# Performance work log

Measured on AMD Instinct MI355X. Metric: run time of the kernel, lower is better.

The kernel has to match this reference:

```python
import jax, jax.numpy as jnp
import numpy as np
from jax import lax

H = 512   # hidden_size
R = 4     # read heads
W = 32    # memory word size
N = 64    # memory cells
B = 64    # batch
T = 256   # seq len
IFACE = R * W + 3 * W + 5 * R + 3      # 247
HID_C = H + IFACE                       # 759 controller LSTM hidden
IN_C = H + R * W                        # 640 controller LSTM input
EPS = 1e-6


def setup_inputs() -> dict:
    key = jax.random.key(0)
    ks = jax.random.split(key, 7)
    s = 0.05
    return {
        "x": jax.random.normal(ks[0], (B, T, H), jnp.float32),
        "Wih_e": jax.random.normal(ks[1], (4 * H, H), jnp.float32) * s,
        "Whh_e": jax.random.normal(ks[2], (4 * H, H), jnp.float32) * s,
        "b_e": jnp.zeros((4 * H,), jnp.float32),
        "Wih_c": jax.random.normal(ks[3], (4 * HID_C, IN_C), jnp.float32) * s,
        "Whh_c": jax.random.normal(ks[4], (4 * HID_C, HID_C), jnp.float32) * s,
        "b_c": jnp.zeros((4 * HID_C,), jnp.float32),
    }


def lstm_cell(xt, h, c, Wih, Whh, b):
    g = xt @ Wih.T + h @ Whh.T + b
    i, f, gg, o = jnp.split(g, 4, axis=-1)  # PyTorch gate order i,f,g,o
    c = jax.nn.sigmoid(f) * c + jax.nn.sigmoid(i) * jnp.tanh(gg)
    h = jax.nn.sigmoid(o) * jnp.tanh(c)
    return h, c


def content_weights(M, keys, strengths):
    # M: [B,N,W], keys: [B,K,W], strengths: [B,K] -> softmaxed similarity [B,K,N]
    Mn = M * lax.rsqrt(jnp.sum(M * M, -1, keepdims=True) + EPS)
    kn = keys * lax.rsqrt(jnp.sum(keys * keys, -1, keepdims=True) + EPS)
    sim = jnp.einsum('bkw,bnw->bkn', kn, Mn)
    return jax.nn.softmax(sim * strengths[..., None], axis=-1)


def reference(x, Wih_e, Whh_e, b_e, Wih_c, Whh_c, b_c):
    # ---- encoder LSTM over time ----
    def enc_step(carry, xt):
        h, c = carry
        h, c = lstm_cell(xt, h, c, Wih_e, Whh_e, b_e)
        return (h, c), h

    z = jnp.zeros((B, H), x.dtype)
    _, enc = lax.scan(enc_step, (z, z), x.transpose(1, 0, 2))  # [T,B,H]

    # ---- controller LSTM + DNC memory per timestep ----
    eye = jnp.eye(N, dtype=x.dtype)

    def dnc_step(carry, e_t):
        h, c, M, u, p, L, wr, ww, rv = carry
        x_t = jnp.concatenate([e_t, rv], axis=-1)          # [B, H + R*W]
        h, c = lstm_cell(x_t, h, c, Wih_c, Whh_c, b_c)
        out = h[:, :H]
        xi = h[:, H:]                                       # [B, IFACE]
        o = 0
        read_keys = jnp.tanh(xi[:, :R * W].reshape(B, R, W)); o = R * W
        read_str = jax.nn.softplus(xi[:, o:o + R]); o += R
        write_key = jnp.tanh(xi[:, o:o + W]).reshape(B, 1, W); o += W
        write_str = jax.nn.softplus(xi[:, o:o + 1]); o += 1
        erase = jax.nn.sigmoid(xi[:, o:o + W]); o += W
        write_vec = jnp.tanh(xi[:, o:o + W]); o += W
        free_g = jax.nn.sigmoid(xi[:, o:o + R]); o += R
        alloc_g = jax.nn.sigmoid(xi[:, o:o + 1]); o += 1
        write_g = jax.nn.sigmoid(xi[:, o:o + 1]); o += 1
        read_modes = jax.nn.softmax(xi[:, o:o + 3 * R].reshape(B, R, 3), -1)
        # usage + retention
        psi = jnp.prod(1.0 - free_g[..., None] * wr, axis=1)   # [B,N]
        u = (u + ww - u * ww) * psi
        # allocation weighting via sorted usage
        idx = jnp.argsort(u, axis=-1)
        su = jnp.take_along_axis(u, idx, -1)
        cp = jnp.concatenate([jnp.ones((B, 1), u.dtype), jnp.cumprod(su, -1)[:, :-1]], -1)
        a = jnp.take_along_axis((1.0 - su) * cp, jnp.argsort(idx, -1), -1)
        # write weighting
        cw = content_weights(M, write_key, write_str)[:, 0]    # [B,N]
        ww = write_g * (alloc_g * a + (1.0 - alloc_g) * cw)
        # memory write
        M = M * (1.0 - ww[..., None] * erase[:, None, :]) + ww[..., None] * write_vec[:, None, :]
        # temporal link + precedence
        L = (1.0 - ww[:, :, None] - ww[:, None, :]) * L + ww[:, :, None] * p[:, None, :]
        L = L * (1.0 - eye)
        p = (1.0 - jnp.sum(ww, -1, keepdims=True)) * p + ww
        # read weighting: backward, content, forward modes
        cr = content_weights(M, read_keys, read_str)           # [B,R,N]
        fw = jnp.einsum('bnm,brm->brn', L, wr)
        bw = jnp.einsum('bmn,brm->brn', L, wr)
        wr = read_modes[..., 0:1] * bw + read_modes[..., 1:2] * cr + read_modes[..., 2:3] * fw
        rv = jnp.einsum('brn,bnw->brw', wr, M).reshape(B, R * W)
        return (h, c, M, u, p, L, wr, ww, rv), out

    init = (
        jnp.zeros((B, HID_C), x.dtype), jnp.zeros((B, HID_C), x.dtype),
        jnp.zeros((B, N, W), x.dtype), jnp.zeros((B, N), x.dtype),
        jnp.zeros((B, N), x.dtype), jnp.zeros((B, N, N), x.dtype),
        jnp.zeros((B, R, N), x.dtype), jnp.zeros((B, N), x.dtype),
        jnp.zeros((B, R * W), x.dtype),
    )
    _, outs = lax.scan(dnc_step, init, enc)   # [T,B,H]
    return outs.transpose(1, 0, 2)            # dnc_encoded [B,T,H]
```

## Files before the change

kernel.cpp:

```cpp
#include <hip/hip_runtime.h>
#include <math.h>


#define EPSF 1e-6f

__device__ __forceinline__ float sigmoidf_(float x) { return 1.f / (1.f + expf(-x)); }
__device__ __forceinline__ float softplusf_(float x) {
    return (x > 0.f) ? x + log1pf(expf(-x)) : log1pf(expf(x));
}
__device__ __forceinline__ void stg_coh(float* p, float v) {
    __hip_atomic_store(p, v, __ATOMIC_RELAXED, __HIP_MEMORY_SCOPE_AGENT);
}
__device__ __forceinline__ void st_flag(int* p, int v) {
    __hip_atomic_store(p, v, __ATOMIC_RELAXED, __HIP_MEMORY_SCOPE_AGENT);
}
__device__ __forceinline__ int ld_flag(const int* p) {
    return __hip_atomic_load(p, __ATOMIC_RELAXED, __HIP_MEMORY_SCOPE_AGENT);
}
__device__ __forceinline__ void poll256(const int* f, int lane, int tgt) {
    const int* p = f + lane * 32;
    for (;;) {
        int a = ld_flag(p);
        int b = ld_flag(p + 64 * 32);
        int c = ld_flag(p + 128 * 32);
        int d = ld_flag(p + 192 * 32);
        if (__all(min(min(a, b), min(c, d)) >= tgt)) break;
        __builtin_amdgcn_s_sleep(2);
    }
}
__device__ __forceinline__ void pollg(const int* f, int lane, int tgt) {
    const int* p = f + (64 + lane) * 32;
    for (;;) {
        int a = ld_flag(p);
        int b = ld_flag(p + 64 * 32);
        int c = ld_flag(p + 128 * 32);
        if (__all(min(min(a, b), c) >= tgt)) break;
        __builtin_amdgcn_s_sleep(2);
    }
}
__device__ __forceinline__ void pollx(const int* f, int lane, int tgt) {
    const int* p = f + (192 + (lane < 62 ? lane : 61)) * 32;
    while (!__all(ld_flag(p) >= tgt)) __builtin_amdgcn_s_sleep(2);
}
__device__ __forceinline__ void pollm(const int* f2, int lane, int tgt) {
    while (!__all(ld_flag(f2 + lane * 32) >= tgt)) __builtin_amdgcn_s_sleep(2);
}

__global__ __launch_bounds__(256) void prep_weights(const float* __restrict__ Whh_c,
                                                    const float* __restrict__ Wih_c,
                                                    float* __restrict__ Wcat) {
    int idx = blockIdx.x * 256 + threadIdx.x;
    if (idx < 3036 * 896) {
        int r = idx / 896, j = idx - r * 896;
        float v;
        if (j < 759) v = Whh_c[r * 759 + j];
        else if (j < 768) v = 0.f;
        else v = Wih_c[r * 640 + 512 + (j - 768)];
        Wcat[idx] = v;
    }
}

__global__ __launch_bounds__(256, 2) void proj_gemm(const float* __restrict__ A,
                                                    const float* __restrict__ W,
                                                    const float* __restrict__ bias,
                                                    float* __restrict__ OUT, int Ncols,
                                                    int wstride, int arow_base, int arow_stride_t,
                                                    int arow_stride_b, int arowlen, int Mrows) {
    __shared__ float As[16 * 68];
    __shared__ float Ws[16 * 68];
    const int tid = threadIdx.x;
    const int ntile = blockIdx.x, mtile = blockIdx.y;
    const int tx = tid & 15, ty = tid >> 4;
    const int lr = tid >> 2;
    const int lk = (tid & 3) * 4;
    const size_t arow =
        (size_t)arow_base + (size_t)mtile * arow_stride_t + (size_t)lr * arow_stride_b;
    const float* aptr = A + arow * arowlen + lk;
    const int wn = ntile * 64 + lr;
    const bool wok = (wn < Ncols);
    const float* wptr = W + (size_t)(wok ? wn : 0) * wstride + lk;
    float acc[4][4] = {};
    for (int kt = 0; kt < 512; kt += 16) {
        float4 av = *(const float4*)(aptr + kt);
        float4 w4l = *(const float4*)(wptr + kt);
        if (!wok) w4l = make_float4(0.f, 0.f, 0.f, 0.f);
        __syncthreads();
        As[(lk + 0) * 68 + lr] = av.x;
        As[(lk + 1) * 68 + lr] = av.y;
        As[(lk + 2) * 68 + lr] = av.z;
        As[(lk + 3) * 68 + lr] = av.w;
        Ws[(lk + 0) * 68 + lr] = w4l.x;
        Ws[(lk + 1) * 68 + lr] = w4l.y;
        Ws[(lk + 2) * 68 + lr] = w4l.z;
        Ws[(lk + 3) * 68 + lr] = w4l.w;
        __syncthreads();
#pragma unroll
        for (int k = 0; k < 16; ++k) {
            float4 a4 = *(const float4*)&As[k * 68 + ty * 4];
            float4 w4 = *(const float4*)&Ws[k * 68 + tx * 4];
            acc[0][0] = fmaf(a4.x, w4.x, acc[0][0]);
            acc[0][1] = fmaf(a4.x, w4.y, acc[0][1]);
            acc[0][2] = fmaf(a4.x, w4.z, acc[0][2]);
            acc[0][3] = fmaf(a4.x, w4.w, acc[0][3]);
            acc[1][0] = fmaf(a4.y, w4.x, acc[1][0]);
            acc[1][1] = fmaf(a4.y, w4.y, acc[1][1]);
            acc[1][2] = fmaf(a4.y, w4.z, acc[1][2]);
            acc[1][3] = fmaf(a4.y, w4.w, acc[1][3]);
            acc[2][0] = fmaf(a4.z, w4.x, acc[2][0]);
            acc[2][1] = fmaf(a4.z, w4.y, acc[2][1]);
            acc[2][2] = fmaf(a4.z, w4.z, acc[2][2]);
            acc[2][3] = fmaf(a4.z, w4.w, acc[2][3]);
            acc[3][0] = fmaf(a4.w, w4.x, acc[3][0]);
            acc[3][1] = fmaf(a4.w, w4.y, acc[3][1]);
            acc[3][2] = fmaf(a4.w, w4.z, acc[3][2]);
            acc[3][3] = fmaf(a4.w, w4.w, acc[3][3]);
        }
    }
    const int col0 = ntile * 64 + tx * 4;
    const int row0 = mtile * 64 + ty * 4;
#pragma unroll
    for (int j = 0; j < 4; ++j) {
        int col = col0 + j;
        if (col < Ncols) {
            float bv = bias[col];
            float4 st = make_float4(acc[0][j] + bv, acc[1][j] + bv, acc[2][j] + bv,
                                    acc[3][j] + bv);
            *(float4*)&OUT[(size_t)col * Mrows + row0] = st;
        }
    }
}

__global__ __launch_bounds__(256) void enc_emit(const float* __restrict__ HSE,
                                                float* __restrict__ ENC, int t0) {
    const int tl = blockIdx.x, bgrp = blockIdx.y;
    const int c4 = threadIdx.x & 127, b = bgrp * 2 + (threadIdx.x >> 7);
    float4 v = *(const float4*)&HSE[(size_t)tl * 32768 + c4 * 256 + b * 4];
    *(float4*)&ENC[((size_t)(t0 + tl) * 64 + b) * 512 + c4 * 4] = v;
}
__global__ __launch_bounds__(256) void out_emit(const float* __restrict__ HS,
                                                float* __restrict__ OUT, int t0) {
    const int tl = blockIdx.x, bgrp = blockIdx.y;
    const int c4 = threadIdx.x & 127, b = bgrp * 2 + (threadIdx.x >> 7);
    float4 v = *(const float4*)&HS[(size_t)tl * 57344 + c4 * 256 + b * 4];
    *(float4*)&OUT[(size_t)b * 131072 + (size_t)(t0 + tl) * 512 + c4 * 4] = v;
}

__global__ __launch_bounds__(512, 1) void enc_seq(const float* __restrict__ Whh,
                                                  const float* __restrict__ XPT,
                                                  float* __restrict__ HSE,
                                                  float* __restrict__ CE, int M, int TC,
                                                  int* flags) {
    __shared__ float part[8 * 4 * 64];
    const int tid = threadIdx.x;
    const int bk = blockIdx.x;
    const int lane = tid & 63;
    const int wv = __builtin_amdgcn_readfirstlane(tid >> 6);
    const int q = wv & 3, cidx = wv >> 2;
    const int cell = bk + 256 * cidx;
    const float* __restrict__ w0 = Whh + ((size_t)(0 * 512 + cell)) * 512 + q * 128;
    const float* __restrict__ w1 = Whh + ((size_t)(1 * 512 + cell)) * 512 + q * 128;
    const float* __restrict__ w2 = Whh + ((size_t)(2 * 512 + cell)) * 512 + q * 128;
    const float* __restrict__ w3 = Whh + ((size_t)(3 * 512 + cell)) * 512 + q * 128;
    float c_reg = 0.f;
    if (q == 0) c_reg = CE[cell * 64 + lane];
    for (int tl = 0; tl < TC; ++tl) {
        const float* rslot = HSE + (size_t)((tl + TC - 1) % TC) * 32768;
        float* wslot = HSE + (size_t)tl * 32768;
        float x0 = 0.f, x1 = 0.f, x2 = 0.f, x3 = 0.f;
        if (q == 0) {
            const int m = tl * 64 + lane;
            x0 = XPT[(size_t)(0 * 512 + cell) * M + m];
            x1 = XPT[(size_t)(1 * 512 + cell) * M + m];
            x2 = XPT[(size_t)(2 * 512 + cell) * M + m];
            x3 = XPT[(size_t)(3 * 512 + cell) * M + m];
        }
        float a0 = 0.f, a1 = 0.f, a2 = 0.f, a3 = 0.f;
        {
            const float4* __restrict__ hx = (const float4*)rslot + q * 32 * 64;
#pragma unroll 8
            for (int i = 0; i < 32; ++i) {
                float4 hv = hx[i * 64 + lane];
                float4 q0 = *(const float4*)&w0[i * 4];
                float4 q1 = *(const float4*)&w1[i * 4];
                float4 q2 = *(const float4*)&w2[i * 4];
                float4 q3 = *(const float4*)&w3[i * 4];
                a0 = fmaf(hv.x, q0.x, a0); a0 = fmaf(hv.y, q0.y, a0);
                a0 = fmaf(hv.z, q0.z, a0); a0 = fmaf(hv.w, q0.w, a0);
                a1 = fmaf(hv.x, q1.x, a1); a1 = fmaf(hv.y, q1.y, a1);
                a1 = fmaf(hv.z, q1.z, a1); a1 = fmaf(hv.w, q1.w, a1);
                a2 = fmaf(hv.x, q2.x, a2); a2 = fmaf(hv.y, q2.y, a2);
                a2 = fmaf(hv.z, q2.z, a2); a2 = fmaf(hv.w, q2.w, a2);
                a3 = fmaf(hv.x, q3.x, a3); a3 = fmaf(hv.y, q3.y, a3);
                a3 = fmaf(hv.z, q3.z, a3); a3 = fmaf(hv.w, q3.w, a3);
            }
        }
        part[(wv * 4 + 0) * 64 + lane] = a0;
        part[(wv * 4 + 1) * 64 + lane] = a1;
        part[(wv * 4 + 2) * 64 + lane] = a2;
        part[(wv * 4 + 3) * 64 + lane] = a3;
        __syncthreads();
        if (q == 0) {
            float g4[4];
#pragma unroll
            for (int g = 0; g < 4; ++g) {
                g4[g] = part[((cidx * 4 + 0) * 4 + g) * 64 + lane] +
                        part[((cidx * 4 + 1) * 4 + g) * 64 + lane] +
                        part[((cidx * 4 + 2) * 4 + g) * 64 + lane] +
                        part[((cidx * 4 + 3) * 4 + g) * 64 + lane];
            }
            float cc = sigmoidf_(g4[1] + x1) * c_reg + sigmoidf_(g4[0] + x0) * tanhf(g4[2] + x2);
            float hh = sigmoidf_(g4[3] + x3) * tanhf(cc);
            c_reg = cc;
            stg_coh(&wslot[(cell >> 2) * 256 + lane * 4 + (cell & 3)], hh);
        }
        __syncthreads();
        if (tid == 0) st_flag(flags + bk * 32, tl + 1);
        if (tl + 1 < TC) {
            if (wv == 0) poll256(flags, lane, tl + 1);
            __syncthreads();
        }
    }
    if (q == 0) CE[cell * 64 + lane] = c_reg;
}

__global__ __launch_bounds__(1024, 1) void dnc_seq(
    const float* __restrict__ Wcat, const float* __restrict__ CPT, float* __restrict__ HS,
    float* __restrict__ CC, float* __restrict__ Mg, float* __restrict__ Ug,
    float* __restrict__ Pg, float* __restrict__ WWg, float* __restrict__ Lg,
    float* __restrict__ WRg, int M, int TC, int* flags) {
    __shared__ float part[16 * 4 * 64];
    __shared__ float M_l[64 * 33];
    __shared__ float L_l[64 * 65];
    __shared__ float act[256];
    __shared__ float wr_l[256];
    __shared__ float u_l[64], p_l[64], ww_l[64], sM2[64], srt_l[64], asrt_l[64];
    __shared__ float modes_l[12], kss_l[4], scal[4];

    const int tid = threadIdx.x;
    const int bk = blockIdx.x;
    const int lane = tid & 63;
    const int wv = __builtin_amdgcn_readfirstlane(tid >> 6);
    const int q = wv & 3, cidx = wv >> 2;
    const bool machb = (bk < 64);
    const int cell_raw = machb ? 0 : (bk - 64) * 4 + cidx;
    const bool valid = !machb && (cell_raw < 759);
    const int cell = valid ? cell_raw : 0;
    const int b = bk;
    int* flags2 = flags + 8192;

    const float* __restrict__ wh0 = Wcat + (size_t)(0 * 759 + cell) * 896 + q * 192;
    const float* __restrict__ wh1 = Wcat + (size_t)(1 * 759 + cell) * 896 + q * 192;
    const float* __restrict__ wh2 = Wcat + (size_t)(2 * 759 + cell) * 896 + q * 192;
    const float* __restrict__ wh3 = Wcat + (size_t)(3 * 759 + cell) * 896 + q * 192;
    const float* __restrict__ wr0 = Wcat + (size_t)(0 * 759 + cell) * 896 + 768 + q * 32;
    const float* __restrict__ wr1 = Wcat + (size_t)(1 * 759 + cell) * 896 + 768 + q * 32;
    const float* __restrict__ wr2 = Wcat + (size_t)(2 * 759 + cell) * 896 + 768 + q * 32;
    const float* __restrict__ wr3 = Wcat + (size_t)(3 * 759 + cell) * 896 + 768 + q * 32;

    float c_reg = 0.f;
    if (valid && q == 0) c_reg = CC[cell * 64 + lane];

    if (machb) {
        if (tid < 256) {
#pragma unroll
            for (int i = 0; i < 8; ++i) {
                int e = tid + 256 * i;
                M_l[(e >> 5) * 33 + (e & 31)] = Mg[b * 2048 + e];
            }
#pragma unroll
            for (int i = 0; i < 16; ++i) {
                int e = tid + 256 * i;
                L_l[(e >> 6) * 65 + (e & 63)] = Lg[b * 4096 + e];
            }
            wr_l[tid] = WRg[b * 256 + tid];
        }
        if (tid < 64) {
            u_l[tid] = Ug[b * 64 + tid];
            p_l[tid] = Pg[b * 64 + tid];
            ww_l[tid] = WWg[b * 64 + tid];
        }
        __syncthreads();
    }

    float cp0 = 0.f, cp1 = 0.f, cp2 = 0.f, cp3 = 0.f;
    if (valid && q == 0) {
        cp0 = CPT[(size_t)(0 * 759 + cell) * M + lane];
        cp1 = CPT[(size_t)(1 * 759 + cell) * M + lane];
        cp2 = CPT[(size_t)(2 * 759 + cell) * M + lane];
        cp3 = CPT[(size_t)(3 * 759 + cell) * M + lane];
    }
    float A0 = 0.f, A1 = 0.f, A2 = 0.f, A3 = 0.f;
    if (valid) {
        const float4* __restrict__ hx = (const float4*)(HS + (size_t)(TC - 1) * 57344) + q * 48 * 64;
#pragma unroll 8
        for (int i = 0; i < 48; ++i) {
            float4 hv = hx[i * 64 + lane];
            float4 u0 = *(const float4*)&wh0[i * 4];
            float4 u1 = *(const float4*)&wh1[i * 4];
            float4 u2 = *(const float4*)&wh2[i * 4];
            float4 u3 = *(const float4*)&wh3[i * 4];
            A0 = fmaf(hv.x, u0.x, A0); A0 = fmaf(hv.y, u0.y, A0);
            A0 = fmaf(hv.z, u0.z, A0); A0 = fmaf(hv.w, u0.w, A0);
            A1 = fmaf(hv.x, u1.x, A1); A1 = fmaf(hv.y, u1.y, A1);
            A1 = fmaf(hv.z, u1.z, A1); A1 = fmaf(hv.w, u1.w, A1);
            A2 = fmaf(hv.x, u2.x, A2); A2 = fmaf(hv.y, u2.y, A2);
            A2 = fmaf(hv.z, u2.z, A2); A2 = fmaf(hv.w, u2.w, A2);
            A3 = fmaf(hv.x, u3.x, A3); A3 = fmaf(hv.y, u3.y, A3);
            A3 = fmaf(hv.z, u3.z, A3); A3 = fmaf(hv.w, u3.w, A3);
        }
    }

    for (int tl = 0; tl < TC; ++tl) {
        const bool last = (tl + 1 == TC);
        const float* rslot = HS + (size_t)((tl + TC - 1) % TC) * 57344;
        float* wslot = HS + (size_t)tl * 57344;
        if (!machb) {
            float b0 = 0.f, b1 = 0.f, b2 = 0.f, b3 = 0.f;
            if (valid) {
                const float4* __restrict__ hx = (const float4*)rslot + (192 + q * 8) * 64;
#pragma unroll
                for (int i = 0; i < 8; ++i) {
                    float4 hv = hx[i * 64 + lane];
                    float4 u0 = *(const float4*)&wr0[i * 4];
                    float4 u1 = *(const float4*)&wr1[i * 4];
                    float4 u2 = *(const float4*)&wr2[i * 4];
                    float4 u3 = *(const float4*)&wr3[i * 4];
                    b0 = fmaf(hv.x, u0.x, b0); b0 = fmaf(hv.y, u0.y, b0);
                    b0 = fmaf(hv.z, u0.z, b0); b0 = fmaf(hv.w, u0.w, b0);
                    b1 = fmaf(hv.x, u1.x, b1); b1 = fmaf(hv.y, u1.y, b1);
                    b1 = fmaf(hv.z, u1.z, b1); b1 = fmaf(hv.w, u1.w, b1);
                    b2 = fmaf(hv.x, u2.x, b2); b2 = fmaf(hv.y, u2.y, b2);
                    b2 = fmaf(hv.z, u2.z, b2); b2 = fmaf(hv.w, u2.w, b2);
                    b3 = fmaf(hv.x, u3.x, b3); b3 = fmaf(hv.y, u3.y, b3);
                    b3 = fmaf(hv.z, u3.z, b3); b3 = fmaf(hv.w, u3.w, b3);
                }
            }
            part[(wv * 4 + 0) * 64 + lane] = A0 + b0;
            part[(wv * 4 + 1) * 64 + lane] = A1 + b1;
            part[(wv * 4 + 2) * 64 + lane] = A2 + b2;
            part[(wv * 4 + 3) * 64 + lane] = A3 + b3;
            __syncthreads();
            if (valid && q == 0) {
                float g4[4];
#pragma unroll
                for (int g = 0; g < 4; ++g) {
                    g4[g] = part[((cidx * 4 + 0) * 4 + g) * 64 + lane] +
                            part[((cidx * 4 + 1) * 4 + g) * 64 + lane] +
                            part[((cidx * 4 + 2) * 4 + g) * 64 + lane] +
                            part[((cidx * 4 + 3) * 4 + g) * 64 + lane];
                }
                float cc =
                    sigmoidf_(g4[1] + cp1) * c_reg + sigmoidf_(g4[0] + cp0) * tanhf(g4[2] + cp2);
                float hh = sigmoidf_(g4[3] + cp3) * tanhf(cc);
                c_reg = cc;
                stg_coh(&wslot[(bk - 64) * 256 + lane * 4 + cidx], hh);
            }
            __syncthreads();
            if (tid == 0) st_flag(flags + bk * 32, tl + 1);
            if (!last) {
                if (wv == 0) pollg(flags, lane, tl + 1);
                __syncthreads();
                float np0 = 0.f, np1 = 0.f, np2 = 0.f, np3 = 0.f;
                if (valid && q == 0) {
                    const int m = (tl + 1) * 64 + lane;
                    np0 = CPT[(size_t)(0 * 759 + cell) * M + m];
                    np1 = CPT[(size_t)(1 * 759 + cell) * M + m];
                    np2 = CPT[(size_t)(2 * 759 + cell) * M + m];
                    np3 = CPT[(size_t)(3 * 759 + cell) * M + m];
                }
                A0 = A1 = A2 = A3 = 0.f;
                if (valid) {
                    const float4* __restrict__ hx = (const float4*)wslot + q * 48 * 64;
#pragma unroll 8
                    for (int i = 0; i < 48; ++i) {
                        float4 hv = hx[i * 64 + lane];
                        float4 u0 = *(const float4*)&wh0[i * 4];
                        float4 u1 = *(const float4*)&wh1[i * 4];
                        float4 u2 = *(const float4*)&wh2[i * 4];
                        float4 u3 = *(const float4*)&wh3[i * 4];
                        A0 = fmaf(hv.x, u0.x, A0); A0 = fmaf(hv.y, u0.y, A0);
                        A0 = fmaf(hv.z, u0.z, A0); A0 = fmaf(hv.w, u0.w, A0);
                        A1 = fmaf(hv.x, u1.x, A1); A1 = fmaf(hv.y, u1.y, A1);
                        A1 = fmaf(hv.z, u1.z, A1); A1 = fmaf(hv.w, u1.w, A1);
                        A2 = fmaf(hv.x, u2.x, A2); A2 = fmaf(hv.y, u2.y, A2);
                        A2 = fmaf(hv.z, u2.z, A2); A2 = fmaf(hv.w, u2.w, A2);
                        A3 = fmaf(hv.x, u3.x, A3); A3 = fmaf(hv.y, u3.y, A3);
                        A3 = fmaf(hv.z, u3.z, A3); A3 = fmaf(hv.w, u3.w, A3);
                    }
                }
                cp0 = np0; cp1 = np1; cp2 = np2; cp3 = np3;
                if (wv == 0) pollm(flags2, lane, tl + 1);
                __syncthreads();
            }
        } else {
            if (wv == 0) pollx(flags, lane, tl + 1);
            __syncthreads();
            if (tid < 247) {
                float v = wslot[(128 + (tid >> 2)) * 256 + b * 4 + (tid & 3)];
                float a;
                if (tid < 128) a = tanhf(v);
                else if (tid < 132) a = softplusf_(v);
                else if (tid < 164) a = tanhf(v);
                else if (tid == 164) a = softplusf_(v);
                else if (tid < 197) a = sigmoidf_(v);
                else if (tid < 229) a = tanhf(v);
                else if (tid < 235) a = sigmoidf_(v);
                else a = v;
                act[tid] = a;
            }
            if (tid < 64) {
                float s2 = 0.f;
                for (int w = 0; w < 32; ++w) {
                    float mm = M_l[tid * 33 + w];
                    s2 = fmaf(mm, mm, s2);
                }
                sM2[tid] = s2;
            }
            __syncthreads();
            if (tid < 64) {
                if (tid < 4) {
                    float m0 = act[235 + 3 * tid], m1 = act[236 + 3 * tid],
                          m2 = act[237 + 3 * tid];
                    float mx = fmaxf(m0, fmaxf(m1, m2));
                    float e0 = expf(m0 - mx), e1 = expf(m1 - mx), e2 = expf(m2 - mx);
                    float s = e0 + e1 + e2;
                    modes_l[3 * tid] = e0 / s;
                    modes_l[3 * tid + 1] = e1 / s;
                    modes_l[3 * tid + 2] = e2 / s;
                    float ks = 0.f;
                    for (int w = 0; w < 32; ++w) {
                        float kk = act[tid * 32 + w];
                        ks = fmaf(kk, kk, ks);
                    }
                    kss_l[tid] = ks;
                }
                if (tid == 4) {
                    float s = 0.f;
                    for (int w = 0; w < 32; ++w) {
                        float kk = act[132 + w];
                        s = fmaf(kk, kk, s);
                    }
                    scal[0] = s;
                }
                float psi = 1.f;
#pragma unroll
                for (int r = 0; r < 4; ++r) psi *= 1.f - act[229 + r] * wr_l[r * 64 + tid];
                float un = u_l[tid], wwo = ww_l[tid];
                float unew = (un + wwo - un * wwo) * psi;
                u_l[tid] = unew;
                int rk = 0;
                for (int m = 0; m < 64; ++m) {
                    float um = u_l[m];
                    rk += (um < unew) || (um == unew && m < tid);
                }
                srt_l[rk] = unew;
                float v = srt_l[tid];
                float incl = v;
#pragma unroll
                for (int off = 1; off < 64; off <<= 1) {
                    float o = __shfl_up(incl, off);
                    if (tid >= off) incl *= o;
                }
                float excl = __shfl_up(incl, 1);
                if (tid == 0) excl = 1.f;
                asrt_l[tid] = (1.f - v) * excl;
                float dot = 0.f;
                for (int w = 0; w < 32; ++w) dot = fmaf(act[132 + w], M_l[tid * 33 + w], dot);
                float logit = dot * rsqrtf(sM2[tid] + EPSF) * rsqrtf(scal[0] + EPSF) * act[164];
                float mx = logit;
#pragma unroll
                for (int off = 32; off; off >>= 1) mx = fmaxf(mx, __shfl_xor(mx, off));
                float e = expf(logit - mx);
                float s = e;
#pragma unroll
                for (int off = 32; off; off >>= 1) s += __shfl_xor(s, off);
                float cw = e / s;
                float a = asrt_l[rk];
                float agv = act[233], wgv = act[234];
                float wn = wgv * (agv * a + (1.f - agv) * cw);
                ww_l[tid] = wn;
                float sw = wn;
#pragma unroll
                for (int off = 32; off; off >>= 1) sw += __shfl_xor(sw, off);
                if (tid == 0) scal[1] = sw;
            }
            __syncthreads();
            if (tid < 256) {
#pragma unroll
                for (int i = 0; i < 8; ++i) {
                    int e = tid + 256 * i;
                    int n = e >> 5, w = e & 31;
                    float wwn = ww_l[n];
                    M_l[n * 33 + w] =
                        M_l[n * 33 + w] * (1.f - wwn * act[165 + w]) + wwn * act[197 + w];
                }
#pragma unroll
                for (int i = 0; i < 16; ++i) {
                    int e = tid + 256 * i;
                    int n = e >> 6, m = e & 63;
                    float Lv = L_l[n * 65 + m];
                    Lv = (1.f - ww_l[n] - ww_l[m]) * Lv + ww_l[n] * p_l[m];
                    L_l[n * 65 + m] = (n == m) ? 0.f : Lv;
                }
            }
            __syncthreads();
            float wrn = 0.f;
            if (tid < 256) {
                const int r = wv;
                const int n = lane;
                if (r == 0) p_l[n] = (1.f - scal[1]) * p_l[n] + ww_l[n];
                float s2 = 0.f;
                for (int w = 0; w < 32; ++w) {
                    float mm = M_l[n * 33 + w];
                    s2 = fmaf(mm, mm, s2);
                }
                float dot = 0.f;
                for (int w = 0; w < 32; ++w) dot = fmaf(act[r * 32 + w], M_l[n * 33 + w], dot);
                float logit = dot * rsqrtf(s2 + EPSF) * rsqrtf(kss_l[r] + EPSF) * act[128 + r];
                float mx = logit;
#pragma unroll
                for (int off = 32; off; off >>= 1) mx = fmaxf(mx, __shfl_xor(mx, off));
                float e = expf(logit - mx);
                float s = e;
#pragma unroll
                for (int off = 32; off; off >>= 1) s += __shfl_xor(s, off);
                float cr = e / s;
                float fw = 0.f, bw = 0.f;
                for (int m = 0; m < 64; ++m) {
                    float wrm = wr_l[r * 64 + m];
                    fw = fmaf(L_l[n * 65 + m], wrm, fw);
                    bw = fmaf(L_l[m * 65 + n], wrm, bw);
                }
                wrn = modes_l[r * 3] * bw + modes_l[r * 3 + 1] * cr + modes_l[r * 3 + 2] * fw;
            }
            __syncthreads();
            if (tid < 256) wr_l[tid] = wrn;
            __syncthreads();
            if (tid < 128) {
                const int r = tid >> 5, w = tid & 31;
                float rv = 0.f;
                for (int n = 0; n < 64; ++n) rv = fmaf(wr_l[r * 64 + n], M_l[n * 33 + w], rv);
                stg_coh(&wslot[(192 + (tid >> 2)) * 256 + b * 4 + (tid & 3)], rv);
            }
            __syncthreads();
            if (tid == 0) st_flag(flags2 + bk * 32, tl + 1);
        }
    }
    if (valid && q == 0) CC[cell * 64 + lane] = c_reg;
    if (machb) {
        if (tid < 256) {
#pragma unroll
            for (int i = 0; i < 8; ++i) {
                int e = tid + 256 * i;
                Mg[b * 2048 + e] = M_l[(e >> 5) * 33 + (e & 31)];
            }
#pragma unroll
            for (int i = 0; i < 16; ++i) {
                int e = tid + 256 * i;
                Lg[b * 4096 + e] = L_l[(e >> 6) * 65 + (e & 63)];
            }
            WRg[b * 256 + tid] = wr_l[tid];
        }
        if (tid < 64) {
            Ug[b * 64 + tid] = u_l[tid];
            Pg[b * 64 + tid] = p_l[tid];
            WWg[b * 64 + tid] = ww_l[tid];
        }
    }
}

extern "C" void kernel_launch(void* const* d_in, const int* in_sizes, int n_in, void* d_out,
                              int out_size, void* d_ws, size_t ws_size, hipStream_t stream) {
    const float* x = (const float*)d_in[0];
    const float* Wih_e = (const float*)d_in[1];
    const float* Whh_e = (const float*)d_in[2];
    const float* b_e = (const float*)d_in[3];
    const float* Wih_c = (const float*)d_in[4];
    const float* Whh_c = (const float*)d_in[5];
    const float* b_c = (const float*)d_in[6];
    float* out = (float*)d_out;
    float* ws = (float*)d_ws;

    int TC = 32;
    while (TC > 2) {
        size_t need =
            ((size_t)11612096 + (size_t)TC * 415488 + (size_t)(512 / TC) * 16384) * 4;
        if (need <= ws_size) break;
        TC >>= 1;
    }
    const int nch = 256 / TC;
    const int M = TC * 64;

    size_t off = 0;
    float* XPT = ws + off; off += (size_t)2048 * M;
    float* CPT = ws + off; off += (size_t)3036 * M;
    float* Wcat = ws + off; off += (size_t)3036 * 896;
    float* ENC = ws + off; off += (size_t)256 * 64 * 512;
    size_t zoff = off;
    float* HSE = ws + off; off += (size_t)TC * 32768;
    float* CE = ws + off; off += 512 * 64;
    float* HS = ws + off; off += (size_t)TC * 57344;
    float* CC = ws + off; off += 759 * 64;
    float* Mg = ws + off; off += 64 * 2048;
    float* Ug = ws + off; off += 64 * 64;
    float* Pg = ws + off; off += 64 * 64;
    float* WWg = ws + off; off += 64 * 64;
    float* Lg = ws + off; off += 64 * 4096;
    float* WRg = ws + off; off += 64 * 256;
    int* BAR = (int*)(ws + off); off += (size_t)2 * nch * 16384;
    size_t zbytes = (off - zoff) * 4;

    hipMemsetAsync(ws + zoff, 0, zbytes, stream);
    prep_weights<<<dim3((3036 * 896 + 255) / 256), dim3(256), 0, stream>>>(Whh_c, Wih_c, Wcat);
    for (int c = 0; c < nch; ++c) {
        proj_gemm<<<dim3(32, TC), dim3(256), 0, stream>>>(x, Wih_e, b_e, XPT, 2048, 512, c * TC,
                                                          1, 256, 512, M);
        enc_seq<<<dim3(256), dim3(512), 0, stream>>>(Whh_e, XPT, HSE, CE, M, TC,
                                                     BAR + (size_t)c * 16384);
        enc_emit<<<dim3(TC, 32), dim3(256), 0, stream>>>(HSE, ENC, c * TC);
    }
    for (int c = 0; c < nch; ++c) {
        proj_gemm<<<dim3(48, TC), dim3(256), 0, stream>>>(ENC, Wih_c, b_c, CPT, 3036, 640,
                                                          c * TC * 64, 64, 1, 512, M);
        dnc_seq<<<dim3(256), dim3(1024), 0, stream>>>(Wcat, CPT, HS, CC, Mg, Ug, Pg, WWg, Lg,
                                                      WRg, M, TC, BAR + (size_t)(nch + c) * 16384);
        out_emit<<<dim3(TC, 32), dim3(256), 0, stream>>>(HS, out, c * TC);
    }
}
```

Baseline: 8.132 ms.

## Fuse encoder chunk k with DNC chunk k-1 in one persistent kernel

Encoder and DNC sequential bodies become device functions that share one union of LDS buffers. A new fused_seq kernel runs DNC blocks for the previous chunk alongside encoder blocks for the current chunk, so the two recurrences overlap instead of running one after the other. Completion flags are also packed densely rather than padded to separate cache lines. The fused kernel needs all 512 blocks of 1024 threads resident at once, with two per CU, which tightens the register budget. That risks spills and, if residency fails, deadlock in the spin barriers. Denser flags may also add contention on shared cache lines.

```diff
diff --git a/kernel.cpp b/kernel.cpp
--- a/kernel.cpp
+++ b/kernel.cpp
@@ -18,33 +18,43 @@
     return __hip_atomic_load(p, __ATOMIC_RELAXED, __HIP_MEMORY_SCOPE_AGENT);
 }
 __device__ __forceinline__ void poll256(const int* f, int lane, int tgt) {
-    const int* p = f + lane * 32;
     for (;;) {
-        int a = ld_flag(p);
-        int b = ld_flag(p + 64 * 32);
-        int c = ld_flag(p + 128 * 32);
-        int d = ld_flag(p + 192 * 32);
+        int a = ld_flag(f + lane);
+        int b = ld_flag(f + 64 + lane);
+        int c = ld_flag(f + 128 + lane);
+        int d = ld_flag(f + 192 + lane);
         if (__all(min(min(a, b), min(c, d)) >= tgt)) break;
         __builtin_amdgcn_s_sleep(2);
     }
 }
 __device__ __forceinline__ void pollg(const int* f, int lane, int tgt) {
-    const int* p = f + (64 + lane) * 32;
     for (;;) {
-        int a = ld_flag(p);
-        int b = ld_flag(p + 64 * 32);
-        int c = ld_flag(p + 128 * 32);
+        int a = ld_flag(f + 64 + lane);
+        int b = ld_flag(f + 128 + lane);
+        int c = ld_flag(f + 192 + lane);
         if (__all(min(min(a, b), c) >= tgt)) break;
         __builtin_amdgcn_s_sleep(2);
     }
 }
 __device__ __forceinline__ void pollx(const int* f, int lane, int tgt) {
-    const int* p = f + (192 + (lane < 62 ? lane : 61)) * 32;
+    const int* p = f + 192 + (lane < 62 ? lane : 61);
     while (!__all(ld_flag(p) >= tgt)) __builtin_amdgcn_s_sleep(2);
 }
 __device__ __forceinline__ void pollm(const int* f2, int lane, int tgt) {
-    while (!__all(ld_flag(f2 + lane * 32) >= tgt)) __builtin_amdgcn_s_sleep(2);
-}
+    while (!__all(ld_flag(f2 + lane) >= tgt)) __builtin_amdgcn_s_sleep(2);
+}
+
+struct EncShared { float part[8 * 4 * 64]; };
+struct DncShared {
+    float part[16 * 4 * 64];
+    float M_l[64 * 33];
+    float L_l[64 * 65];
+    float act[256];
+    float wr_l[256];
+    float u_l[64], p_l[64], ww_l[64], sM2[64], srt_l[64], asrt_l[64];
+    float modes_l[12], kss_l[4], scal[4];
+};
+union FusedShared { EncShared e; DncShared d; };
 
 __global__ __launch_bounds__(256) void prep_weights(const float* __restrict__ Whh_c,
                                                     const float* __restrict__ Wih_c,
@@ -145,37 +155,36 @@
     *(float4*)&OUT[(size_t)b * 131072 + (size_t)(t0 + tl) * 512 + c4 * 4] = v;
 }
 
-__global__ __launch_bounds__(512, 1) void enc_seq(const float* __restrict__ Whh,
-                                                  const float* __restrict__ XPT,
-                                                  float* __restrict__ HSE,
-                                                  float* __restrict__ CE, int M, int TC,
-                                                  int* flags) {
-    __shared__ float part[8 * 4 * 64];
+__device__ void enc_body(int bk, EncShared& sh, const float* __restrict__ Whh,
+                         const float* __restrict__ XPT, float* __restrict__ HSE,
+                         float* __restrict__ CE, int M, int TC, int* flags) {
+    float* part = sh.part;
     const int tid = threadIdx.x;
-    const int bk = blockIdx.x;
     const int lane = tid & 63;
     const int wv = __builtin_amdgcn_readfirstlane(tid >> 6);
-    const int q = wv & 3, cidx = wv >> 2;
+    const bool w8 = (wv < 8);
+    const int q = wv & 3, cidx = (wv >> 2) & 1;
     const int cell = bk + 256 * cidx;
     const float* __restrict__ w0 = Whh + ((size_t)(0 * 512 + cell)) * 512 + q * 128;
     const float* __restrict__ w1 = Whh + ((size_t)(1 * 512 + cell)) * 512 + q * 128;
     const float* __restrict__ w2 = Whh + ((size_t)(2 * 512 + cell)) * 512 + q * 128;
     const float* __restrict__ w3 = Whh + ((size_t)(3 * 512 + cell)) * 512 + q * 128;
+    const bool gw = w8 && (q == 0);
     float c_reg = 0.f;
-    if (q == 0) c_reg = CE[cell * 64 + lane];
+    if (gw) c_reg = CE[cell * 64 + lane];
     for (int tl = 0; tl < TC; ++tl) {
         const float* rslot = HSE + (size_t)((tl + TC - 1) % TC) * 32768;
         float* wslot = HSE + (size_t)tl * 32768;
         float x0 = 0.f, x1 = 0.f, x2 = 0.f, x3 = 0.f;
-        if (q == 0) {
+        if (gw) {
             const int m = tl * 64 + lane;
             x0 = XPT[(size_t)(0 * 512 + cell) * M + m];
             x1 = XPT[(size_t)(1 * 512 + cell) * M + m];
             x2 = XPT[(size_t)(2 * 512 + cell) * M + m];
             x3 = XPT[(size_t)(3 * 512 + cell) * M + m];
         }
-        float a0 = 0.f, a1 = 0.f, a2 = 0.f, a3 = 0.f;
-        {
+        if (w8) {
+            float a0 = 0.f, a1 = 0.f, a2 = 0.f, a3 = 0.f;
             const float4* __restrict__ hx = (const float4*)rslot + q * 32 * 64;
 #pragma unroll 8
             for (int i = 0; i < 32; ++i) {
@@ -193,13 +202,13 @@
                 a3 = fmaf(hv.x, q3.x, a3); a3 = fmaf(hv.y, q3.y, a3);
                 a3 = fmaf(hv.z, q3.z, a3); a3 = fmaf(hv.w, q3.w, a3);
             }
-        }
-        part[(wv * 4 + 0) * 64 + lane] = a0;
-        part[(wv * 4 + 1) * 64 + lane] = a1;
-        part[(wv * 4 + 2) * 64 + lane] = a2;
-        part[(wv * 4 + 3) * 64 + lane] = a3;
+            part[(wv * 4 + 0) * 64 + lane] = a0;
+            part[(wv * 4 + 1) * 64 + lane] = a1;
+            part[(wv * 4 + 2) * 64 + lane] = a2;
+            part[(wv * 4 + 3) * 64 + lane] = a3;
+        }
         __syncthreads();
-        if (q == 0) {
+        if (gw) {
             float g4[4];
 #pragma unroll
             for (int g = 0; g < 4; ++g) {
@@ -214,30 +223,37 @@
             stg_coh(&wslot[(cell >> 2) * 256 + lane * 4 + (cell & 3)], hh);
         }
         __syncthreads();
-        if (tid == 0) st_flag(flags + bk * 32, tl + 1);
+        if (tid == 0) st_flag(flags + bk, tl + 1);
         if (tl + 1 < TC) {
             if (wv == 0) poll256(flags, lane, tl + 1);
             __syncthreads();
         }
     }
-    if (q == 0) CE[cell * 64 + lane] = c_reg;
-}
-
-__global__ __launch_bounds__(1024, 1) void dnc_seq(
-    const float* __restrict__ Wcat, const float* __restrict__ CPT, float* __restrict__ HS,
-    float* __restrict__ CC, float* __restrict__ Mg, float* __restrict__ Ug,
-    float* __restrict__ Pg, float* __restrict__ WWg, float* __restrict__ Lg,
-    float* __restrict__ WRg, int M, int TC, int* flags) {
-    __shared__ float part[16 * 4 * 64];
-    __shared__ float M_l[64 * 33];
-    __shared__ float L_l[64 * 65];
-    __shared__ float act[256];
-    __shared__ float wr_l[256];
-    __shared__ float u_l[64], p_l[64], ww_l[64], sM2[64], srt_l[64], asrt_l[64];
-    __shared__ float modes_l[12], kss_l[4], scal[4];
+    if (gw) CE[cell * 64 + lane] = c_reg;
+}
+
+__device__ void dnc_body(int bk, DncShared& sh, const float* __restrict__ Wcat,
+                         const float* __restrict__ CPT, float* __restrict__ HS,
+                         float* __restrict__ CC, float* __restrict__ Mg,
+                         float* __restrict__ Ug, float* __restrict__ Pg,
+                         float* __restrict__ WWg, float* __restrict__ Lg,
+                         float* __restrict__ WRg, int M, int TC, int* flags) {
+    float* part = sh.part;
+    float* M_l = sh.M_l;
+    float* L_l = sh.L_l;
+    float* act = sh.act;
+    float* wr_l = sh.wr_l;
+    float* u_l = sh.u_l;
+    float* p_l = sh.p_l;
+    float* ww_l = sh.ww_l;
+    float* sM2 = sh.sM2;
+    float* srt_l = sh.srt_l;
+    float* asrt_l = sh.asrt_l;
+    float* modes_l = sh.modes_l;
+    float* kss_l = sh.kss_l;
+    float* scal = sh.scal;
 
     const int tid = threadIdx.x;
-    const int bk = blockIdx.x;
     const int lane = tid & 63;
     const int wv = __builtin_amdgcn_readfirstlane(tid >> 6);
     const int q = wv & 3, cidx = wv >> 2;
@@ -282,6 +298,26 @@
         __syncthreads();
     }
 
+#define ACC768_R6(SLOT)                                                              \
+    {                                                                                \
+        const float4* __restrict__ hx = (const float4*)(SLOT) + q * 48 * 64;         \
+        _Pragma("unroll 8") for (int i = 0; i < 48; ++i) {                           \
+            float4 hv = hx[i * 64 + lane];                                           \
+            float4 u0 = *(const float4*)&wh0[i * 4];                                 \
+            float4 u1 = *(const float4*)&wh1[i * 4];                                 \
+            float4 u2 = *(const float4*)&wh2[i * 4];                                 \
+            float4 u3 = *(const float4*)&wh3[i * 4];                                 \
+            A0 = fmaf(hv.x, u0.x, A0); A0 = fmaf(hv.y, u0.y, A0);                    \
+            A0 = fmaf(hv.z, u0.z, A0); A0 = fmaf(hv.w, u0.w, A0);                    \
+            A1 = fmaf(hv.x, u1.x, A1); A1 = fmaf(hv.y, u1.y, A1);                    \
+            A1 = fmaf(hv.z, u1.z, A1); A1 = fmaf(hv.w, u1.w, A1);                    \
+            A2 = fmaf(hv.x, u2.x, A2); A2 = fmaf(hv.y, u2.y, A2);                    \
+            A2 = fmaf(hv.z, u2.z, A2); A2 = fmaf(hv.w, u2.w, A2);                    \
+            A3 = fmaf(hv.x, u3.x, A3); A3 = fmaf(hv.y, u3.y, A3);                    \
+            A3 = fmaf(hv.z, u3.z, A3); A3 = fmaf(hv.w, u3.w, A3);                    \
+        }                                                                            \
+    }
+
     float cp0 = 0.f, cp1 = 0.f, cp2 = 0.f, cp3 = 0.f;
     if (valid && q == 0) {
         cp0 = CPT[(size_t)(0 * 759 + cell) * M + lane];
@@ -290,25 +326,7 @@
         cp3 = CPT[(size_t)(3 * 759 + cell) * M + lane];
     }
     float A0 = 0.f, A1 = 0.f, A2 = 0.f, A3 = 0.f;
-    if (valid) {
-        const float4* __restrict__ hx = (const float4*)(HS + (size_t)(TC - 1) * 57344) + q * 48 * 64;
-#pragma unroll 8
-        for (int i = 0; i < 48; ++i) {
-            float4 hv = hx[i * 64 + lane];
-            float4 u0 = *(const float4*)&wh0[i * 4];
-            float4 u1 = *(const float4*)&wh1[i * 4];
-            float4 u2 = *(const float4*)&wh2[i * 4];
-            float4 u3 = *(const float4*)&wh3[i * 4];
-            A0 = fmaf(hv.x, u0.x, A0); A0 = fmaf(hv.y, u0.y, A0);
-            A0 = fmaf(hv.z, u0.z, A0); A0 = fmaf(hv.w, u0.w, A0);
-            A1 = fmaf(hv.x, u1.x, A1); A1 = fmaf(hv.y, u1.y, A1);
-            A1 = fmaf(hv.z, u1.z, A1); A1 = fmaf(hv.w, u1.w, A1);
-            A2 = fmaf(hv.x, u2.x, A2); A2 = fmaf(hv.y, u2.y, A2);
-            A2 = fmaf(hv.z, u2.z, A2); A2 = fmaf(hv.w, u2.w, A2);
-            A3 = fmaf(hv.x, u3.x, A3); A3 = fmaf(hv.y, u3.y, A3);
-            A3 = fmaf(hv.z, u3.z, A3); A3 = fmaf(hv.w, u3.w, A3);
-        }
-    }
+    if (valid) ACC768_R6(HS + (size_t)(TC - 1) * 57344);
 
     for (int tl = 0; tl < TC; ++tl) {
         const bool last = (tl + 1 == TC);
@@ -356,7 +374,7 @@
                 stg_coh(&wslot[(bk - 64) * 256 + lane * 4 + cidx], hh);
             }
             __syncthreads();
-            if (tid == 0) st_flag(flags + bk * 32, tl + 1);
+            if (tid == 0) st_flag(flags + bk, tl + 1);
             if (!last) {
                 if (wv == 0) pollg(flags, lane, tl + 1);
                 __syncthreads();
@@ -369,25 +387,7 @@
                     np3 = CPT[(size_t)(3 * 759 + cell) * M + m];
                 }
                 A0 = A1 = A2 = A3 = 0.f;
-                if (valid) {
-                    const float4* __restrict__ hx = (const float4*)wslot + q * 48 * 64;
-#pragma unroll 8
-                    for (int i = 0; i < 48; ++i) {
-                        float4 hv = hx[i * 64 + lane];
-                        float4 u0 = *(const float4*)&wh0[i * 4];
-                        float4 u1 = *(const float4*)&wh1[i * 4];
-                        float4 u2 = *(const float4*)&wh2[i * 4];
-                        float4 u3 = *(const float4*)&wh3[i * 4];
-                        A0 = fmaf(hv.x, u0.x, A0); A0 = fmaf(hv.y, u0.y, A0);
-                        A0 = fmaf(hv.z, u0.z, A0); A0 = fmaf(hv.w, u0.w, A0);
-                        A1 = fmaf(hv.x, u1.x, A1); A1 = fmaf(hv.y, u1.y, A1);
-                        A1 = fmaf(hv.z, u1.z, A1); A1 = fmaf(hv.w, u1.w, A1);
-                        A2 = fmaf(hv.x, u2.x, A2); A2 = fmaf(hv.y, u2.y, A2);
-                        A2 = fmaf(hv.z, u2.z, A2); A2 = fmaf(hv.w, u2.w, A2);
-                        A3 = fmaf(hv.x, u3.x, A3); A3 = fmaf(hv.y, u3.y, A3);
-                        A3 = fmaf(hv.z, u3.z, A3); A3 = fmaf(hv.w, u3.w, A3);
-                    }
-                }
+                if (valid) ACC768_R6(wslot);
                 cp0 = np0; cp1 = np1; cp2 = np2; cp3 = np3;
                 if (wv == 0) pollm(flags2, lane, tl + 1);
                 __syncthreads();
@@ -423,10 +423,10 @@
                           m2 = act[237 + 3 * tid];
                     float mx = fmaxf(m0, fmaxf(m1, m2));
                     float e0 = expf(m0 - mx), e1 = expf(m1 - mx), e2 = expf(m2 - mx);
-                    float s = e0 + e1 + e2;
-                    modes_l[3 * tid] = e0 / s;
-                    modes_l[3 * tid + 1] = e1 / s;
-                    modes_l[3 * tid + 2] = e2 / s;
+                    float sm = e0 + e1 + e2;
+                    modes_l[3 * tid] = e0 / sm;
+                    modes_l[3 * tid + 1] = e1 / sm;
+                    modes_l[3 * tid + 2] = e2 / sm;
                     float ks = 0.f;
                     for (int w = 0; w < 32; ++w) {
                         float kk = act[tid * 32 + w];
@@ -435,12 +435,12 @@
                     kss_l[tid] = ks;
                 }
                 if (tid == 4) {
-                    float s = 0.f;
+                    float sm = 0.f;
                     for (int w = 0; w < 32; ++w) {
                         float kk = act[132 + w];
-                        s = fmaf(kk, kk, s);
+                        sm = fmaf(kk, kk, sm);
                     }
-                    scal[0] = s;
+                    scal[0] = sm;
                 }
                 float psi = 1.f;
 #pragma unroll
@@ -471,10 +471,10 @@
 #pragma unroll
                 for (int off = 32; off; off >>= 1) mx = fmaxf(mx, __shfl_xor(mx, off));
                 float e = expf(logit - mx);
-                float s = e;
-#pragma unroll
-                for (int off = 32; off; off >>= 1) s += __shfl_xor(s, off);
-                float cw = e / s;
+                float sm = e;
+#pragma unroll
+                for (int off = 32; off; off >>= 1) sm += __shfl_xor(sm, off);
+                float cw = e / sm;
                 float a = asrt_l[rk];
                 float agv = act[233], wgv = act[234];
                 float wn = wgv * (agv * a + (1.f - agv) * cw);
@@ -521,10 +521,10 @@
 #pragma unroll
                 for (int off = 32; off; off >>= 1) mx = fmaxf(mx, __shfl_xor(mx, off));
                 float e = expf(logit - mx);
-                float s = e;
-#pragma unroll
-                for (int off = 32; off; off >>= 1) s += __shfl_xor(s, off);
-                float cr = e / s;
+                float sm = e;
+#pragma unroll
+                for (int off = 32; off; off >>= 1) sm += __shfl_xor(sm, off);
+                float cr = e / sm;
                 float fw = 0.f, bw = 0.f;
                 for (int m = 0; m < 64; ++m) {
                     float wrm = wr_l[r * 64 + m];
@@ -543,7 +543,7 @@
                 stg_coh(&wslot[(192 + (tid >> 2)) * 256 + b * 4 + (tid & 3)], rv);
             }
             __syncthreads();
-            if (tid == 0) st_flag(flags2 + bk * 32, tl + 1);
+            if (tid == 0) st_flag(flags2 + bk, tl + 1);
         }
     }
     if (valid && q == 0) CC[cell * 64 + lane] = c_reg;
@@ -566,6 +566,40 @@
             Pg[b * 64 + tid] = p_l[tid];
             WWg[b * 64 + tid] = ww_l[tid];
         }
+    }
+#undef ACC768_R6
+}
+
+__global__ __launch_bounds__(512, 1) void enc_seq(const float* __restrict__ Whh,
+                                                  const float* __restrict__ XPT,
+                                                  float* __restrict__ HSE,
+                                                  float* __restrict__ CE, int M, int TC,
+                                                  int* flags) {
+    __shared__ EncShared sh;
+    enc_body(blockIdx.x, sh, Whh, XPT, HSE, CE, M, TC, flags);
+}
+
+__global__ __launch_bounds__(1024, 1) void dnc_seq(
+    const float* __restrict__ Wcat, const float* __restrict__ CPT, float* __restrict__ HS,
+    float* __restrict__ CC, float* __restrict__ Mg, float* __restrict__ Ug,
+    float* __restrict__ Pg, float* __restrict__ WWg, float* __restrict__ Lg,
+    float* __restrict__ WRg, int M, int TC, int* flags) {
+    __shared__ DncShared sh;
+    dnc_body(blockIdx.x, sh, Wcat, CPT, HS, CC, Mg, Ug, Pg, WWg, Lg, WRg, M, TC, flags);
+}
+
+__global__ __launch_bounds__(1024, 8) void fused_seq(
+    const float* __restrict__ Whh_e, const float* __restrict__ XPT, float* __restrict__ HSE,
+    float* __restrict__ CE, const float* __restrict__ Wcat, const float* __restrict__ CPT,
+    float* __restrict__ HS, float* __restrict__ CC, float* __restrict__ Mg,
+    float* __restrict__ Ug, float* __restrict__ Pg, float* __restrict__ WWg,
+    float* __restrict__ Lg, float* __restrict__ WRg, int M, int TC, int* eflags,
+    int* dflags) {
+    __shared__ FusedShared sh;
+    if (blockIdx.x < 256) {
+        dnc_body(blockIdx.x, sh.d, Wcat, CPT, HS, CC, Mg, Ug, Pg, WWg, Lg, WRg, M, TC, dflags);
+    } else {
+        enc_body(blockIdx.x - 256, sh.e, Whh_e, XPT, HSE, CE, M, TC, eflags);
     }
 }
 
@@ -612,18 +646,25 @@
 
     hipMemsetAsync(ws + zoff, 0, zbytes, stream);
     prep_weights<<<dim3((3036 * 896 + 255) / 256), dim3(256), 0, stream>>>(Whh_c, Wih_c, Wcat);
-    for (int c = 0; c < nch; ++c) {
-        proj_gemm<<<dim3(32, TC), dim3(256), 0, stream>>>(x, Wih_e, b_e, XPT, 2048, 512, c * TC,
+
+    proj_gemm<<<dim3(32, TC), dim3(256), 0, stream>>>(x, Wih_e, b_e, XPT, 2048, 512, 0, 1, 256,
+                                                      512, M);
+    enc_seq<<<dim3(256), dim3(512), 0, stream>>>(Whh_e, XPT, HSE, CE, M, TC, BAR);
+    enc_emit<<<dim3(TC, 32), dim3(256), 0, stream>>>(HSE, ENC, 0);
+    for (int k = 1; k < nch; ++k) {
+        proj_gemm<<<dim3(32, TC), dim3(256), 0, stream>>>(x, Wih_e, b_e, XPT, 2048, 512, k * TC,
                                                           1, 256, 512, M);
-        enc_seq<<<dim3(256), dim3(512), 0, stream>>>(Whh_e, XPT, HSE, CE, M, TC,
-                                                     BAR + (size_t)c * 16384);
-        enc_emit<<<dim3(TC, 32), dim3(256), 0, stream>>>(HSE, ENC, c * TC);
-    }
-    for (int c = 0; c < nch; ++c) {
         proj_gemm<<<dim3(48, TC), dim3(256), 0, stream>>>(ENC, Wih_c, b_c, CPT, 3036, 640,
-                                                          c * TC * 64, 64, 1, 512, M);
-        dnc_seq<<<dim3(256), dim3(1024), 0, stream>>>(Wcat, CPT, HS, CC, Mg, Ug, Pg, WWg, Lg,
-                                                      WRg, M, TC, BAR + (size_t)(nch + c) * 16384);
-        out_emit<<<dim3(TC, 32), dim3(256), 0, stream>>>(HS, out, c * TC);
-    }
-}
+                                                          (k - 1) * TC * 64, 64, 1, 512, M);
+        fused_seq<<<dim3(512), dim3(1024), 0, stream>>>(
+            Whh_e, XPT, HSE, CE, Wcat, CPT, HS, CC, Mg, Ug, Pg, WWg, Lg, WRg, M, TC,
+            BAR + (size_t)k * 16384, BAR + (size_t)(nch + k - 1) * 16384);
+        enc_emit<<<dim3(TC, 32), dim3(256), 0, stream>>>(HSE, ENC, k * TC);
+        out_emit<<<dim3(TC, 32), dim3(256), 0, stream>>>(HS, out, (k - 1) * TC);
+    }
+    proj_gemm<<<dim3(48, TC), dim3(256), 0, stream>>>(ENC, Wih_c, b_c, CPT, 3036, 640,
+                                                      (nch - 1) * TC * 64, 64, 1, 512, M);
+    dnc_seq<<<dim3(256), dim3(1024), 0, stream>>>(Wcat, CPT, HS, CC, Mg, Ug, Pg, WWg, Lg, WRg,
+                                                  M, TC, BAR + (size_t)(2 * nch - 1) * 16384);
+    out_emit<<<dim3(TC, 32), dim3(256), 0, stream>>>(HS, out, (nch - 1) * TC);
+}
```

New measurement: 16.61 ms. +104.2%, slower.
